# Performance work log

Hardware: AMD Instinct MI355X
Metric: run time of the kernel (lower is better)

## Reference

```python
import jax, jax.numpy as jnp
from jax import lax
import numpy as np

HIDDEN = 50


def setup_inputs() -> dict:
    key = jax.random.key(0)
    ks = jax.random.split(key, 7)
    B, T, I, H, O = 2048, 512, 1, HIDDEN, 1
    s = 1.0 / np.sqrt(H)  # PyTorch nn.RNN init scale (uniform); we use normal*s for simplicity
    return {
        "x": jax.random.normal(ks[0], (B, T, I), dtype=jnp.float32),
        "W_ih": jax.random.normal(ks[1], (H, I), dtype=jnp.float32) * s,
        "W_hh": jax.random.normal(ks[2], (H, H), dtype=jnp.float32) * s,
        "b_ih": jax.random.normal(ks[3], (H,), dtype=jnp.float32) * s,
        "b_hh": jax.random.normal(ks[4], (H,), dtype=jnp.float32) * s,
        "W_fc": jax.random.normal(ks[5], (O, H), dtype=jnp.float32) * s,
        "b_fc": jax.random.normal(ks[6], (O,), dtype=jnp.float32) * s,
    }


def reference(x, W_ih, W_hh, b_ih, b_hh, W_fc, b_fc):
    # Vanilla tanh RNN (batch_first), h0 = 0; return fc(h_T).
    B = x.shape[0]
    H = W_hh.shape[0]
    # Precompute input projections for all timesteps: [T, B, H]
    xproj = jnp.einsum("bti,hi->tbh", x, W_ih) + b_ih

    def step(h, xt):
        h_new = jnp.tanh(xt + h @ W_hh.T + b_hh)
        return h_new, None

    h0 = jnp.zeros((B, H), dtype=x.dtype)
    hT, _ = lax.scan(step, h0, xproj)
    return hT @ W_fc.T + b_fc  # [B, 1]
```

## Files before the change

### kernel.cpp

```cpp
#include <hip/hip_runtime.h>

#define HID 50
#define TSTEPS 512

typedef float f32x2 __attribute__((ext_vector_type(2)));
typedef float f32x4 __attribute__((ext_vector_type(4)));

__global__ __launch_bounds__(64) __attribute__((amdgpu_waves_per_eu(2, 2)))
void rnn_fused(
    const float* __restrict__ x,
    const float* __restrict__ W_ih,
    const float* __restrict__ W_hh,
    const float* __restrict__ b_ih,
    const float* __restrict__ b_hh,
    const float* __restrict__ W_fc,
    const float* __restrict__ b_fc,
    float* __restrict__ out)
{
    const int b = blockIdx.x;
    const int j = threadIdx.x;
    __shared__ __align__(16) float hlds[64];
    __shared__ __align__(16) float xbuf[64];

    const int jj = (j < HID) ? j : 0;
    const float SC = 2.8853900817779268f;

    f32x2 w2[26];
#pragma unroll
    for (int m = 0; m < 25; ++m) {
        f32x2 t;
        t.x = W_hh[jj * HID + 2 * m]     * SC;
        t.y = W_hh[jj * HID + 2 * m + 1] * SC;
        w2[m] = t;
    }
    w2[25] = (f32x2)(0.0f);

    const float wih  = W_ih[jj] * SC;
    const float btot = (b_ih[jj] + b_hh[jj]) * SC;
    const float wfc  = (j < HID) ? W_fc[jj] : 0.0f;
    const float bfc  = b_fc[0];

    const float* xb = x + (size_t)b * TSTEPS;
    float xv = xb[j];
    float hn = 0.0f;
    hlds[j] = 0.0f;
    __syncthreads();

    for (int c = 0; c < TSTEPS / 64; ++c) {
        xbuf[j] = xv;
        float xv_next = 0.0f;
        if (c + 1 < TSTEPS / 64) xv_next = xb[(c + 1) * 64 + j];
        __syncthreads();

        for (int g = 0; g < 8; ++g) {
#pragma unroll
            for (int ii = 0; ii < 8; ++ii) {
                const int t = g * 8 + ii;
                const float xt  = xbuf[t];
                const float xtc = fmaf(xt, wih, btot);

                const f32x4* h4 = (const f32x4*)hlds;
                f32x2 a0 = (f32x2)(0.0f), a1 = (f32x2)(0.0f);
                f32x2 a2 = (f32x2)(0.0f), a3 = (f32x2)(0.0f);
#pragma unroll
                for (int q = 0; q < 13; ++q) {
                    const f32x4 p = h4[q];
                    const f32x2 plo = __builtin_shufflevector(p, p, 0, 1);
                    const f32x2 phi = __builtin_shufflevector(p, p, 2, 3);
                    if ((q & 1) == 0) {
                        a0 = __builtin_elementwise_fma(plo, w2[2 * q],     a0);
                        a1 = __builtin_elementwise_fma(phi, w2[2 * q + 1], a1);
                    } else {
                        a2 = __builtin_elementwise_fma(plo, w2[2 * q],     a2);
                        a3 = __builtin_elementwise_fma(phi, w2[2 * q + 1], a3);
                    }
                }
                a0 = a0 + a1;
                a2 = a2 + a3;
                a0 = a0 + a2;
                const float z = (a0.x + a0.y) + xtc;

                const float e = __builtin_amdgcn_exp2f(z);
                const float r = __builtin_amdgcn_rcpf(e + 1.0f);
                hn = fmaf(-2.0f, r, 1.0f);

                hlds[j] = hn;
                __syncthreads();
            }
        }
        xv = xv_next;
    }

    float pr = hn * wfc;
#pragma unroll
    for (int off = 32; off >= 1; off >>= 1) pr += __shfl_xor(pr, off);
    if (j == 0) out[b] = pr + bfc;
}

extern "C" void kernel_launch(void* const* d_in, const int* in_sizes, int n_in,
                              void* d_out, int out_size, void* d_ws, size_t ws_size,
                              hipStream_t stream) {
    (void)d_ws; (void)ws_size; (void)n_in; (void)out_size;
    const float* x    = (const float*)d_in[0];
    const float* W_ih = (const float*)d_in[1];
    const float* W_hh = (const float*)d_in[2];
    const float* b_ih = (const float*)d_in[3];
    const float* b_hh = (const float*)d_in[4];
    const float* W_fc = (const float*)d_in[5];
    const float* b_fc = (const float*)d_in[6];
    float* out = (float*)d_out;

    const int B = in_sizes[0] / TSTEPS;
    rnn_fused<<<dim3(B), dim3(64), 0, stream>>>(x, W_ih, W_hh, b_ih, b_hh, W_fc, b_fc, out);
}
```

Measured before the change: 120.9 us.

## Drop block barriers for single-wavefront RNN step and use scalar FMAs

```diff
diff --git a/kernel.cpp b/kernel.cpp
--- a/kernel.cpp
+++ b/kernel.cpp
@@ -3,7 +3,6 @@
 #define HID 50
 #define TSTEPS 512
 
-typedef float f32x2 __attribute__((ext_vector_type(2)));
 typedef float f32x4 __attribute__((ext_vector_type(4)));
 
 __global__ __launch_bounds__(64) __attribute__((amdgpu_waves_per_eu(2, 2)))
@@ -25,15 +24,11 @@
     const int jj = (j < HID) ? j : 0;
     const float SC = 2.8853900817779268f;
 
-    f32x2 w2[26];
+    float w[52];
 #pragma unroll
-    for (int m = 0; m < 25; ++m) {
-        f32x2 t;
-        t.x = W_hh[jj * HID + 2 * m]     * SC;
-        t.y = W_hh[jj * HID + 2 * m + 1] * SC;
-        w2[m] = t;
-    }
-    w2[25] = (f32x2)(0.0f);
+    for (int k = 0; k < HID; ++k) w[k] = W_hh[jj * HID + k] * SC;
+    w[50] = 0.0f;
+    w[51] = 0.0f;
 
     const float wih  = W_ih[jj] * SC;
     const float btot = (b_ih[jj] + b_hh[jj]) * SC;
@@ -43,49 +38,36 @@
     const float* xb = x + (size_t)b * TSTEPS;
     float xv = xb[j];
     float hn = 0.0f;
-    hlds[j] = 0.0f;
-    __syncthreads();
 
     for (int c = 0; c < TSTEPS / 64; ++c) {
         xbuf[j] = xv;
         float xv_next = 0.0f;
         if (c + 1 < TSTEPS / 64) xv_next = xb[(c + 1) * 64 + j];
-        __syncthreads();
 
         for (int g = 0; g < 8; ++g) {
 #pragma unroll
             for (int ii = 0; ii < 8; ++ii) {
                 const int t = g * 8 + ii;
-                const float xt  = xbuf[t];
+
+                hlds[j] = hn;
+                const float xt = xbuf[t];
                 const float xtc = fmaf(xt, wih, btot);
 
                 const f32x4* h4 = (const f32x4*)hlds;
-                f32x2 a0 = (f32x2)(0.0f), a1 = (f32x2)(0.0f);
-                f32x2 a2 = (f32x2)(0.0f), a3 = (f32x2)(0.0f);
+                float a0 = xtc, a1 = 0.0f, a2 = 0.0f, a3 = 0.0f;
 #pragma unroll
                 for (int q = 0; q < 13; ++q) {
                     const f32x4 p = h4[q];
-                    const f32x2 plo = __builtin_shufflevector(p, p, 0, 1);
-                    const f32x2 phi = __builtin_shufflevector(p, p, 2, 3);
-                    if ((q & 1) == 0) {
-                        a0 = __builtin_elementwise_fma(plo, w2[2 * q],     a0);
-                        a1 = __builtin_elementwise_fma(phi, w2[2 * q + 1], a1);
-                    } else {
-                        a2 = __builtin_elementwise_fma(plo, w2[2 * q],     a2);
-                        a3 = __builtin_elementwise_fma(phi, w2[2 * q + 1], a3);
-                    }
+                    a0 = fmaf(p.x, w[4 * q + 0], a0);
+                    a1 = fmaf(p.y, w[4 * q + 1], a1);
+                    a2 = fmaf(p.z, w[4 * q + 2], a2);
+                    a3 = fmaf(p.w, w[4 * q + 3], a3);
                 }
-                a0 = a0 + a1;
-                a2 = a2 + a3;
-                a0 = a0 + a2;
-                const float z = (a0.x + a0.y) + xtc;
+                const float z = (a0 + a1) + (a2 + a3);
 
                 const float e = __builtin_amdgcn_exp2f(z);
                 const float r = __builtin_amdgcn_rcpf(e + 1.0f);
                 hn = fmaf(-2.0f, r, 1.0f);
-
-                hlds[j] = hn;
-                __syncthreads();
             }
         }
         xv = xv_next;
```

Measured after the change: 152.2 us. 25.9% more time.
